# Kernel tuning notes

Hardware: AMD Instinct MI355X
Metric: run time of the kernel (lower is better)

## Reference

```python
import jax, jax.numpy as jnp
import numpy as np

B = 4096          # graphs (frames)
NPG = 22          # players per frame
N = B * NPG       # total nodes
E = B * NPG * (NPG - 1)
D_BB = 256        # backbone_dout == GRNN hidden
D_NODE = 128      # raw node feature dim
D_PROJ = 256      # cfg.proj_dout
D_GIN = 64        # glob_din
D_GOUT = 128      # cfg.glob_dout
D_IN = D_BB + D_PROJ  # GRNN input dim = 512


def setup_inputs() -> dict:
    key = jax.random.key(0)
    ks = jax.random.split(key, 24)
    def w(k, shape):
        return jax.random.normal(k, shape, jnp.float32) * 0.05
    inp = {
        "z": jax.random.normal(ks[0], (N, D_BB), jnp.float32),
        "u": jax.random.normal(ks[1], (B, D_GIN), jnp.float32),
        "x": jax.random.normal(ks[2], (N, D_NODE), jnp.float32),
        # edge_index is unused math-wise because GConvGRU is built with K=1 ChebConvs
        "edge_index": jax.random.randint(ks[3], (2, E), 0, N, dtype=jnp.int32),
        "batch": jnp.repeat(jnp.arange(B, dtype=jnp.int32), NPG),
        "batch_size": B,
        "prev_h": jax.random.normal(ks[4], (N, D_BB), jnp.float32),
        # fusion params
        "w_proj": w(ks[5], (D_NODE, D_PROJ)), "b_proj": jnp.zeros((D_PROJ,), jnp.float32),
        "w_glob": w(ks[6], (D_GIN, D_GOUT)), "b_glob": jnp.zeros((D_GOUT,), jnp.float32),
        # GConvGRU (K=1 ChebConv == linear) gate params: update z, reset r, candidate h
        "W_xz": w(ks[7], (D_IN, D_BB)),  "b_xz": jnp.zeros((D_BB,), jnp.float32),
        "W_hz": w(ks[8], (D_BB, D_BB)),  "b_hz": jnp.zeros((D_BB,), jnp.float32),
        "W_xr": w(ks[9], (D_IN, D_BB)),  "b_xr": jnp.zeros((D_BB,), jnp.float32),
        "W_hr": w(ks[10], (D_BB, D_BB)), "b_hr": jnp.zeros((D_BB,), jnp.float32),
        "W_xh": w(ks[11], (D_IN, D_BB)), "b_xh": jnp.zeros((D_BB,), jnp.float32),
        "W_hh": w(ks[12], (D_BB, D_BB)), "b_hh": jnp.zeros((D_BB,), jnp.float32),
    }
    return inp


def reference(z, u, x, edge_index, batch, batch_size, prev_h,
              w_proj, b_proj, w_glob, b_glob,
              W_xz, b_xz, W_hz, b_hz,
              W_xr, b_xr, W_hr, b_hr,
              W_xh, b_xh, W_hh, b_hh):
    # --- GraphGlobalFusion: mean readout + relu(Linear(u)) + concat ---
    sums = jax.ops.segment_sum(z, batch, num_segments=batch_size)            # [B, D_BB]
    cnts = jax.ops.segment_sum(jnp.ones((z.shape[0], 1), z.dtype), batch,
                               num_segments=batch_size)                      # [B, 1]
    graph_emb = sums / jnp.maximum(cnts, 1.0)
    glob_emb = jax.nn.relu(u @ w_glob + b_glob)                              # [B, D_GOUT]
    fused = jnp.concatenate([graph_emb, glob_emb], axis=-1)                  # [B, D_BB+D_GOUT]

    # --- node mode: raw feature projection, then GConvGRU (K=1 -> linear gates) ---
    x_proj = jax.nn.relu(x @ w_proj + b_proj)                                # [N, D_PROJ]
    xin = jnp.concatenate([z, x_proj], axis=-1)                              # [N, D_IN]
    Z = jax.nn.sigmoid(xin @ W_xz + b_xz + prev_h @ W_hz + b_hz)
    R = jax.nn.sigmoid(xin @ W_xr + b_xr + prev_h @ W_hr + b_hr)
    H_tilde = jnp.tanh(xin @ W_xh + b_xh + (prev_h * R) @ W_hh + b_hh)
    h = Z * prev_h + (1.0 - Z) * H_tilde                                     # [N, D_BB]
    return (fused, h)
```

## Files before the change

### kernel.cpp

```cpp
#include <hip/hip_runtime.h>
#include <hip/hip_bf16.h>

#define NNODES 90112
#define BGRAPH 4096
#define NPG 22
#define DBB 256
#define DNODE 128
#define DPROJ 256
#define DGIN 64
#define DGOUT 128

#define WTG_OFF   32768
#define WTHH_OFF  622592
#define WS_BF16_ELEMS 688128

typedef __attribute__((ext_vector_type(8))) short bf16x8;
typedef __attribute__((ext_vector_type(4))) short bf16x4;
typedef __attribute__((ext_vector_type(4))) float f32x4;

__device__ __forceinline__ short f2bf(float f) {
  __hip_bfloat16 h = __float2bfloat16(f);
  return *reinterpret_cast<short*>(&h);
}
__device__ __forceinline__ float bf2f(short s) {
  union { unsigned int u; float f; } c;
  c.u = ((unsigned int)(unsigned short)s) << 16;
  return c.f;
}
__device__ __forceinline__ float fsig(float xv) {
  return __fdividef(1.0f, 1.0f + __expf(-xv));
}
__device__ __forceinline__ float ftanh(float xv) {
  return 1.0f - __fdividef(2.0f, __expf(2.0f * xv) + 1.0f);
}
__device__ __forceinline__ bf16x8 pack8(f32x4 a, f32x4 b) {
  bf16x8 o;
  o[0]=f2bf(a[0]); o[1]=f2bf(a[1]); o[2]=f2bf(a[2]); o[3]=f2bf(a[3]);
  o[4]=f2bf(b[0]); o[5]=f2bf(b[1]); o[6]=f2bf(b[2]); o[7]=f2bf(b[3]);
  return o;
}

#define DMA16(gsrc, ldst)                                                        \
  __builtin_amdgcn_global_load_lds(                                              \
      (const __attribute__((address_space(1))) void*)(gsrc),                     \
      (__attribute__((address_space(3))) void*)(ldst), 16, 0, 0)

#define GLF(dst, p) asm volatile("global_load_dwordx4 %0, %1, off"               \
                                 : "=&v"(dst) : "v"(p) : "memory")

template<int N>
__device__ __forceinline__ void vmwaitN() {
  static_assert(N >= 0 && N <= 8, "vmcnt range");
  if constexpr (N == 0) asm volatile("s_waitcnt vmcnt(0)" ::: "memory");
  else if constexpr (N == 1) asm volatile("s_waitcnt vmcnt(1)" ::: "memory");
  else if constexpr (N == 2) asm volatile("s_waitcnt vmcnt(2)" ::: "memory");
  else if constexpr (N == 3) asm volatile("s_waitcnt vmcnt(3)" ::: "memory");
  else if constexpr (N == 4) asm volatile("s_waitcnt vmcnt(4)" ::: "memory");
  else if constexpr (N == 5) asm volatile("s_waitcnt vmcnt(5)" ::: "memory");
  else if constexpr (N == 6) asm volatile("s_waitcnt vmcnt(6)" ::: "memory");
  else if constexpr (N == 7) asm volatile("s_waitcnt vmcnt(7)" ::: "memory");
  else asm volatile("s_waitcnt vmcnt(8)" ::: "memory");
  __builtin_amdgcn_sched_barrier(0);
}
#define LBAR() do { asm volatile("s_waitcnt lgkmcnt(0)" ::: "memory");           \
                    __builtin_amdgcn_s_barrier(); } while (0)

__global__ void pack_weights(const float* __restrict__ w_proj,
                             const float* __restrict__ W_xz, const float* __restrict__ W_hz,
                             const float* __restrict__ W_xr, const float* __restrict__ W_hr,
                             const float* __restrict__ W_xh, const float* __restrict__ W_hh,
                             const float* __restrict__ b_xz, const float* __restrict__ b_hz,
                             const float* __restrict__ b_xr, const float* __restrict__ b_hr,
                             const float* __restrict__ b_xh, const float* __restrict__ b_hh,
                             __hip_bfloat16* __restrict__ wsb, float* __restrict__ wsf) {
  int i = blockIdx.x * 256 + threadIdx.x;
  if (i < 32768) {
    int c = i >> 7, k = i & 127;
    wsb[i] = __float2bfloat16(w_proj[k * DPROJ + c]);
  } else if (i < WTHH_OFF) {
    int j = i - WTG_OFF;
    int kc  = j / 24576;
    int rem = j - kc * 24576;
    int ct  = rem >> 9;
    int q   = rem & 511;
    int l   = q >> 3, e = q & 7;
    int l15 = l & 15, kg = l >> 4;
    int k   = kc * 32 + kg * 8 + e;
    int g   = ct >> 4;
    int c   = (ct & 15) * 16 + l15;
    float v;
    if (g == 0)      v = (k < 512) ? W_xz[k * 256 + c] : W_hz[(k - 512) * 256 + c];
    else if (g == 1) v = (k < 512) ? W_xr[k * 256 + c] : W_hr[(k - 512) * 256 + c];
    else             v = (k < 512) ? W_xh[k * 256 + c] : 0.0f;
    wsb[i] = __float2bfloat16(v);
  } else if (i < WS_BF16_ELEMS) {
    int j = i - WTHH_OFF;
    int kc  = j >> 13;
    int rem = j & 8191;
    int ct  = rem >> 9;
    int q   = rem & 511;
    int l   = q >> 3, e = q & 7;
    int l15 = l & 15, kg = l >> 4;
    int k   = kc * 32 + kg * 8 + e;
    int c   = ct * 16 + l15;
    wsb[i] = __float2bfloat16(W_hh[k * 256 + c]);
  }
  if (i < 256) {
    wsf[i]       = b_xz[i] + b_hz[i];
    wsf[256 + i] = b_xr[i] + b_hr[i];
    wsf[512 + i] = b_xh[i] + b_hh[i];
  }
}

__global__ void fused_head(const float* __restrict__ z, const float* __restrict__ u,
                           const float* __restrict__ w_glob, const float* __restrict__ b_glob,
                           float* __restrict__ out) {
  int b = blockIdx.x;
  int t = threadIdx.x;
  __shared__ float us[DGIN];
  if (t < DGIN) us[t] = u[b * DGIN + t];
  __syncthreads();
  const float* zb = z + (size_t)b * NPG * DBB;
  #pragma unroll
  for (int half = 0; half < 2; ++half) {
    int c = t + half * 128;
    float s = 0.f;
    #pragma unroll
    for (int r = 0; r < NPG; ++r) s += zb[r * DBB + c];
    out[(size_t)b * 384 + c] = s * (1.0f / NPG);
  }
  float acc = b_glob[t];
  #pragma unroll
  for (int k = 0; k < DGIN; ++k) acc += us[k] * w_glob[k * DGOUT + t];
  out[(size_t)b * 384 + 256 + t] = fmaxf(acc, 0.f);
}

#define MFMA16(a, b, c) __builtin_amdgcn_mfma_f32_16x16x32_bf16(a, b, c, 0, 0, 0)

template<int KC>
__device__ __forceinline__ void gstep(
    const __hip_bfloat16* __restrict__ wpk, __hip_bfloat16* Wb,
    const __hip_bfloat16* Av, const __hip_bfloat16* XP,
    int l15, int lg, int wid, int lane,
    f32x4 (&accz)[4], f32x4 (&accr)[4], f32x4 (&acch)[4]) {
  constexpr bool has_h = (KC < 16);
  constexpr int NW = (KC <= 8) ? 3
                   : (KC == 9 || KC == 10 || KC == 12 || KC == 13) ? 5
                   : (KC == 11 || KC == 14) ? 3
                   : (KC <= 22) ? 2 : 0;
  const __hip_bfloat16* ab = (KC >= 8 && KC < 16) ? XP : Av;
  const int gk = (KC & 7) * 4 + lg;
  bf16x8 act[4];
  #pragma unroll
  for (int rt = 0; rt < 4; ++rt) {
    const int row = rt * 16 + l15;
    act[rt] = *(const bf16x8*)(ab + row * 256 + ((gk ^ (row & 7)) * 8));
  }
  vmwaitN<NW>();
  bf16x8 wz = *(const bf16x8*)&Wb[((KC & 1) * 3 + 0) * 8192 + wid * 512 + lane * 8];
  bf16x8 wr = *(const bf16x8*)&Wb[((KC & 1) * 3 + 1) * 8192 + wid * 512 + lane * 8];
  bf16x8 wh;
  if constexpr (has_h)
    wh = *(const bf16x8*)&Wb[((KC & 1) * 3 + 2) * 8192 + wid * 512 + lane * 8];
  __builtin_amdgcn_s_setprio(1);
  #pragma unroll
  for (int rt = 0; rt < 4; ++rt) {
    accz[rt] = MFMA16(wz, act[rt], accz[rt]);
    accr[rt] = MFMA16(wr, act[rt], accr[rt]);
    if constexpr (has_h) acch[rt] = MFMA16(wh, act[rt], acch[rt]);
  }
  __builtin_amdgcn_s_setprio(0);
  if constexpr (KC + 2 <= 23) {
    constexpr int ns = ((KC + 2) < 16) ? 3 : 2;
    #pragma unroll
    for (int g = 0; g < 3; ++g)
      if (g < ns)
        DMA16(wpk + (((size_t)(KC + 2) * 48 + g * 16 + wid) * 64 + lane) * 8,
              Wb + (((KC + 2) & 1) * 3 + g) * 8192 + wid * 512);
  }
}

template<int S>
__device__ __forceinline__ void hstep(
    const __hip_bfloat16* __restrict__ hpk, __hip_bfloat16* Wb, __hip_bfloat16* XP,
    int l15, int lg, int wid, int lane, f32x4 (&acch)[4]) {
  constexpr int NW = (S <= 5) ? 2 : (S == 6) ? 1 : 0;
  bf16x8 act[4];
  #pragma unroll
  for (int rt = 0; rt < 4; ++rt) {
    const int row = rt * 16 + l15;
    const int gk = S * 4 + lg;
    act[rt] = *(const bf16x8*)&XP[row * 256 + ((gk ^ (row & 7)) * 8)];
  }
  vmwaitN<NW>();
  bf16x8 w = *(const bf16x8*)&Wb[(S % 4) * 8192 + wid * 512 + lane * 8];
  __builtin_amdgcn_s_setprio(1);
  #pragma unroll
  for (int rt = 0; rt < 4; ++rt) acch[rt] = MFMA16(w, act[rt], acch[rt]);
  __builtin_amdgcn_s_setprio(0);
  if constexpr (S + 3 <= 7)
    DMA16(hpk + (((size_t)(S + 3) * 16 + wid) * 64 + lane) * 8,
          Wb + ((S + 3) % 4) * 8192 + wid * 512);
}

__global__ __launch_bounds__(1024)
void grnn_main(const float* __restrict__ z, const float* __restrict__ x,
               const float* __restrict__ prev_h, const float* __restrict__ b_proj,
               const __hip_bfloat16* __restrict__ wsb, const float* __restrict__ wsf,
               float* __restrict__ h_out) {
  __shared__ __align__(16) __hip_bfloat16 Wb[6 * 8192];
  __shared__ __align__(16) __hip_bfloat16 Av[64 * 256];
  __shared__ __align__(16) __hip_bfloat16 XP[64 * 256];

  const int r0   = blockIdx.x * 64;
  const int tid  = threadIdx.x;
  const int wid  = tid >> 6;
  const int lane = tid & 63;
  const int l15  = lane & 15;
  const int lg   = lane >> 4;
  const int c0   = wid * 16;
  const int cgrp = (c0 >> 3) + (lg >> 1);
  const int lgl  = (lg & 1) * 4;
  const int prow = tid >> 4;
  const int pg   = tid & 15;

  const __hip_bfloat16* wpk = wsb + WTG_OFF;
  const __hip_bfloat16* hpk = wsb + WTHH_OFF;

  {
    const float* p = x + (size_t)(r0 + prow) * DNODE + pg * 8;
    f32x4 f0 = *(const f32x4*)p;
    f32x4 f1 = *(const f32x4*)(p + 4);
    *(bf16x8*)&XP[prow * 128 + ((pg ^ (prow & 7)) * 8)] = pack8(f0, f1);
  }
  __syncthreads();

  f32x4 z0, z1, z2, z3;
  {
    const float* zb = z + (size_t)(r0 + prow) * DBB + pg * 16;
    z0 = *(const f32x4*)zb;       z1 = *(const f32x4*)(zb + 4);
    z2 = *(const f32x4*)(zb + 8); z3 = *(const f32x4*)(zb + 12);
  }
  f32x4 accp[4] = {};
  {
    const __hip_bfloat16* wp0 = wsb + (size_t)(c0 + l15) * DNODE + lg * 8;
    #pragma unroll
    for (int kb = 0; kb < 4; ++kb) {
      bf16x8 wp = *(const bf16x8*)(wp0 + kb * 32);
      const int gk = kb * 4 + lg;
      bf16x8 act[4];
      #pragma unroll
      for (int rt = 0; rt < 4; ++rt) {
        const int row = rt * 16 + l15;
        act[rt] = *(const bf16x8*)&XP[row * 128 + ((gk ^ (row & 7)) * 8)];
      }
      __builtin_amdgcn_s_setprio(1);
      #pragma unroll
      for (int rt = 0; rt < 4; ++rt)
        accp[rt] = MFMA16(wp, act[rt], accp[rt]);
      __builtin_amdgcn_s_setprio(0);
    }
  }
  #pragma unroll
  for (int c = 0; c < 2; ++c)
    #pragma unroll
    for (int g = 0; g < 3; ++g)
      DMA16(wpk + (((size_t)c * 48 + g * 16 + wid) * 64 + lane) * 8,
            Wb + ((c & 1) * 3 + g) * 8192 + wid * 512);
  LBAR();
  {
    float4 bp4 = *(const float4*)&b_proj[c0 + lg * 4];
    #pragma unroll
    for (int rt = 0; rt < 4; ++rt) {
      int r = rt * 16 + l15;
      bf16x4 o;
      o[0] = f2bf(fmaxf(accp[rt][0] + bp4.x, 0.f));
      o[1] = f2bf(fmaxf(accp[rt][1] + bp4.y, 0.f));
      o[2] = f2bf(fmaxf(accp[rt][2] + bp4.z, 0.f));
      o[3] = f2bf(fmaxf(accp[rt][3] + bp4.w, 0.f));
      *(bf16x4*)&XP[r * 256 + ((cgrp ^ (r & 7)) * 8) + lgl] = o;
    }
  }
  *(bf16x8*)&Av[prow * 256 + (((2 * pg) ^ (prow & 7)) * 8)]     = pack8(z0, z1);
  *(bf16x8*)&Av[prow * 256 + (((2 * pg + 1) ^ (prow & 7)) * 8)] = pack8(z2, z3);
  LBAR();

  f32x4 accz[4] = {}, accr[4] = {}, acch[4] = {};
  const float* phb = prev_h + (size_t)(r0 + prow) * DBB + pg * 8;
  f32x4 pa0, pa1, pb0, pb1;
  #define GS(K) gstep<K>(wpk, Wb, Av, XP, l15, lg, wid, lane, accz, accr, acch)
  GS(0); GS(1); GS(2); GS(3); GS(4); GS(5); GS(6); GS(7);
  LBAR();
  GS(8);
  GLF(pa0, phb); GLF(pa1, phb + 4);
  GS(9); GS(10);
  vmwaitN<6>();
  *(bf16x8*)&Av[prow * 256 + ((pg ^ (prow & 7)) * 8)] = pack8(pa0, pa1);
  GS(11);
  GLF(pb0, phb + 128); GLF(pb1, phb + 132);
  GS(12); GS(13);
  vmwaitN<6>();
  *(bf16x8*)&Av[prow * 256 + (((16 + pg) ^ (prow & 7)) * 8)] = pack8(pb0, pb1);
  GS(14); GS(15);
  LBAR();
  GS(16); GS(17); GS(18); GS(19); GS(20); GS(21); GS(22); GS(23);
  #undef GS

  #pragma unroll
  for (int s = 0; s < 3; ++s)
    DMA16(hpk + (((size_t)s * 16 + wid) * 64 + lane) * 8, Wb + (s % 4) * 8192 + wid * 512);
  {
    float4 br4 = *(const float4*)&wsf[256 + c0 + lg * 4];
    #pragma unroll
    for (int rt = 0; rt < 4; ++rt) {
      int r = rt * 16 + l15;
      int off = r * 256 + ((cgrp ^ (r & 7)) * 8) + lgl;
      bf16x4 p4 = *(const bf16x4*)&Av[off];
      bf16x4 o;
      o[0] = f2bf(bf2f(p4[0]) * fsig(accr[rt][0] + br4.x));
      o[1] = f2bf(bf2f(p4[1]) * fsig(accr[rt][1] + br4.y));
      o[2] = f2bf(bf2f(p4[2]) * fsig(accr[rt][2] + br4.z));
      o[3] = f2bf(bf2f(p4[3]) * fsig(accr[rt][3] + br4.w));
      *(bf16x4*)&XP[off] = o;
    }
  }
  LBAR();

  #define HS(S) hstep<S>(hpk, Wb, XP, l15, lg, wid, lane, acch)
  HS(0); HS(1); HS(2); HS(3); HS(4); HS(5); HS(6); HS(7);
  #undef HS

  {
    float4 bz4 = *(const float4*)&wsf[c0 + lg * 4];
    float4 bh4 = *(const float4*)&wsf[512 + c0 + lg * 4];
    #pragma unroll
    for (int rt = 0; rt < 4; ++rt) {
      int r = rt * 16 + l15;
      bf16x4 p4 = *(const bf16x4*)&Av[r * 256 + ((cgrp ^ (r & 7)) * 8) + lgl];
      f32x4 hv;
      float zg = fsig(accz[rt][0] + bz4.x);
      hv[0] = zg * bf2f(p4[0]) + (1.f - zg) * ftanh(acch[rt][0] + bh4.x);
      zg = fsig(accz[rt][1] + bz4.y);
      hv[1] = zg * bf2f(p4[1]) + (1.f - zg) * ftanh(acch[rt][1] + bh4.y);
      zg = fsig(accz[rt][2] + bz4.z);
      hv[2] = zg * bf2f(p4[2]) + (1.f - zg) * ftanh(acch[rt][2] + bh4.z);
      zg = fsig(accz[rt][3] + bz4.w);
      hv[3] = zg * bf2f(p4[3]) + (1.f - zg) * ftanh(acch[rt][3] + bh4.w);
      *(f32x4*)&h_out[(size_t)(r0 + r) * DBB + c0 + lg * 4] = hv;
    }
  }
}

extern "C" void kernel_launch(void* const* d_in, const int* in_sizes, int n_in,
                              void* d_out, int out_size, void* d_ws, size_t ws_size,
                              hipStream_t stream) {
  const float* z      = (const float*)d_in[0];
  const float* u      = (const float*)d_in[1];
  const float* x      = (const float*)d_in[2];
  const float* prev_h = (const float*)d_in[6];
  const float* w_proj = (const float*)d_in[7];
  const float* b_proj = (const float*)d_in[8];
  const float* w_glob = (const float*)d_in[9];
  const float* b_glob = (const float*)d_in[10];
  const float* W_xz   = (const float*)d_in[11];
  const float* b_xz   = (const float*)d_in[12];
  const float* W_hz   = (const float*)d_in[13];
  const float* b_hz   = (const float*)d_in[14];
  const float* W_xr   = (const float*)d_in[15];
  const float* b_xr   = (const float*)d_in[16];
  const float* W_hr   = (const float*)d_in[17];
  const float* b_hr   = (const float*)d_in[18];
  const float* W_xh   = (const float*)d_in[19];
  const float* b_xh   = (const float*)d_in[20];
  const float* W_hh   = (const float*)d_in[21];
  const float* b_hh   = (const float*)d_in[22];

  __hip_bfloat16* wsb = (__hip_bfloat16*)d_ws;
  float* wsf = (float*)((char*)d_ws + (size_t)WS_BF16_ELEMS * 2);

  float* fused = (float*)d_out;
  float* h_out = fused + (size_t)BGRAPH * 384;

  pack_weights<<<dim3(WS_BF16_ELEMS / 256), dim3(256), 0, stream>>>(
      w_proj, W_xz, W_hz, W_xr, W_hr, W_xh, W_hh,
      b_xz, b_hz, b_xr, b_hr, b_xh, b_hh, wsb, wsf);

  fused_head<<<dim3(BGRAPH), dim3(128), 0, stream>>>(z, u, w_glob, b_glob, fused);

  grnn_main<<<dim3(NNODES / 64), dim3(1024), 0, stream>>>(
      z, x, prev_h, b_proj, wsb, wsf, h_out);
}
```

Before: 195.9 us.

## Fuse graph mean readout into GRNN kernel using staged bf16 tile and atomics

The per-graph mean of z is now computed inside grnn_main from the bf16 z tile already staged in shared memory and accumulated into the fused output with atomicAdd. The head kernel only zero-initialises that region and computes the global MLP. This removes a second full read of z from global memory. In exchange the sums are taken over bf16-rounded values, which lowers precision, and graphs that straddle tile boundaries need float atomics, which makes the summation order nondeterministic.

```diff
diff --git a/kernel.cpp b/kernel.cpp
--- a/kernel.cpp
+++ b/kernel.cpp
@@ -17,6 +17,7 @@
 typedef __attribute__((ext_vector_type(8))) short bf16x8;
 typedef __attribute__((ext_vector_type(4))) short bf16x4;
 typedef __attribute__((ext_vector_type(4))) float f32x4;
+typedef __attribute__((ext_vector_type(2))) float f32x2;
 
 __device__ __forceinline__ short f2bf(float f) {
   __hip_bfloat16 h = __float2bfloat16(f);
@@ -112,23 +113,16 @@
   }
 }
 
-__global__ void fused_head(const float* __restrict__ z, const float* __restrict__ u,
-                           const float* __restrict__ w_glob, const float* __restrict__ b_glob,
-                           float* __restrict__ out) {
+__global__ void head_init(const float* __restrict__ u,
+                          const float* __restrict__ w_glob, const float* __restrict__ b_glob,
+                          float* __restrict__ out) {
   int b = blockIdx.x;
   int t = threadIdx.x;
   __shared__ float us[DGIN];
   if (t < DGIN) us[t] = u[b * DGIN + t];
+  f32x2 zz = {0.f, 0.f};
+  *(f32x2*)&out[(size_t)b * 384 + t * 2] = zz;
   __syncthreads();
-  const float* zb = z + (size_t)b * NPG * DBB;
-  #pragma unroll
-  for (int half = 0; half < 2; ++half) {
-    int c = t + half * 128;
-    float s = 0.f;
-    #pragma unroll
-    for (int r = 0; r < NPG; ++r) s += zb[r * DBB + c];
-    out[(size_t)b * 384 + c] = s * (1.0f / NPG);
-  }
   float acc = b_glob[t];
   #pragma unroll
   for (int k = 0; k < DGIN; ++k) acc += us[k] * w_glob[k * DGOUT + t];
@@ -207,7 +201,7 @@
 void grnn_main(const float* __restrict__ z, const float* __restrict__ x,
                const float* __restrict__ prev_h, const float* __restrict__ b_proj,
                const __hip_bfloat16* __restrict__ wsb, const float* __restrict__ wsf,
-               float* __restrict__ h_out) {
+               float* __restrict__ fused, float* __restrict__ h_out) {
   __shared__ __align__(16) __hip_bfloat16 Wb[6 * 8192];
   __shared__ __align__(16) __hip_bfloat16 Av[64 * 256];
   __shared__ __align__(16) __hip_bfloat16 XP[64 * 256];
@@ -284,6 +278,23 @@
   *(bf16x8*)&Av[prow * 256 + (((2 * pg) ^ (prow & 7)) * 8)]     = pack8(z0, z1);
   *(bf16x8*)&Av[prow * 256 + (((2 * pg + 1) ^ (prow & 7)) * 8)] = pack8(z2, z3);
   LBAR();
+
+  {
+    const int gl = tid >> 8;
+    const int c  = tid & 255;
+    const int g  = r0 / NPG + gl;
+    if (g < BGRAPH) {
+      int lo = g * NPG - r0;      if (lo < 0) lo = 0;
+      int hi = g * NPG + NPG - r0; if (hi > 64) hi = 64;
+      if (lo < hi) {
+        const int cg = c >> 3, ce = c & 7;
+        float s = 0.f;
+        for (int row = lo; row < hi; ++row)
+          s += bf2f(*(const short*)&Av[row * 256 + (((cg ^ (row & 7)) << 3) + ce)]);
+        atomicAdd(&fused[(size_t)g * 384 + c], s * (1.0f / NPG));
+      }
+    }
+  }
 
   f32x4 accz[4] = {}, accr[4] = {}, acch[4] = {};
   const float* phb = prev_h + (size_t)(r0 + prow) * DBB + pg * 8;
@@ -385,8 +396,8 @@
       w_proj, W_xz, W_hz, W_xr, W_hr, W_xh, W_hh,
       b_xz, b_hz, b_xr, b_hr, b_xh, b_hh, wsb, wsf);
 
-  fused_head<<<dim3(BGRAPH), dim3(128), 0, stream>>>(z, u, w_glob, b_glob, fused);
+  head_init<<<dim3(BGRAPH), dim3(128), 0, stream>>>(u, w_glob, b_glob, fused);
 
   grnn_main<<<dim3(NNODES / 64), dim3(1024), 0, stream>>>(
-      z, x, prev_h, b_proj, wsb, wsf, h_out);
-}
+      z, x, prev_h, b_proj, wsb, wsf, fused, h_out);
+}
```

Measured after the change: 208.6 us. 6.4% more time.

## Compute per-graph z partial sums inside GRNN kernel from LDS-staged z

Applied to the files above, without the earlier changes.

The graph mean readout no longer re-reads z from global memory in a separate kernel. The GRNN kernel sums the bf16 z rows it has already staged in shared memory into per-block, per-graph partial sums in workspace, and a small head kernel combines at most two partials per graph. This saves a full pass over z (about 92 MB of fp32 reads) but computes the mean from bf16-rounded z, which adds some precision error. It also adds a serial shared-memory reduction step inside the main kernel.

```diff
diff --git a/kernel.cpp b/kernel.cpp
--- a/kernel.cpp
+++ b/kernel.cpp
@@ -9,14 +9,19 @@
 #define DPROJ 256
 #define DGIN 64
 #define DGOUT 128
+#define NBLK (NNODES / 64)
 
 #define WTG_OFF   32768
 #define WTHH_OFF  622592
 #define WS_BF16_ELEMS 688128
+#define WS2_BYTE_OFF ((size_t)WS_BF16_ELEMS * 2 + 768 * 4)
+#define WS2_BYTES    ((size_t)NBLK * 4 * 256 * 4)
+#define WS_NEED      (WS2_BYTE_OFF + WS2_BYTES)
 
 typedef __attribute__((ext_vector_type(8))) short bf16x8;
 typedef __attribute__((ext_vector_type(4))) short bf16x4;
 typedef __attribute__((ext_vector_type(4))) float f32x4;
+typedef __attribute__((ext_vector_type(2))) float f32x2;
 
 __device__ __forceinline__ short f2bf(float f) {
   __hip_bfloat16 h = __float2bfloat16(f);
@@ -135,6 +140,33 @@
   out[(size_t)b * 384 + 256 + t] = fmaxf(acc, 0.f);
 }
 
+__global__ void head2(const float* __restrict__ u,
+                      const float* __restrict__ w_glob, const float* __restrict__ b_glob,
+                      const float* __restrict__ ws2, float* __restrict__ out) {
+  int b = blockIdx.x;
+  int t = threadIdx.x;
+  __shared__ float us[DGIN];
+  if (t < DGIN) us[t] = u[b * DGIN + t];
+  __syncthreads();
+  const int rlo = b * NPG, rhi = b * NPG + NPG - 1;
+  const int b0 = rlo >> 6, b1 = rhi >> 6;
+  const int gl0 = b - (b0 * 64) / NPG;
+  #pragma unroll
+  for (int half = 0; half < 2; ++half) {
+    int c = t + half * 128;
+    float s = ws2[((size_t)b0 * 4 + gl0) * 256 + c];
+    if (b1 != b0) {
+      const int gl1 = b - (b1 * 64) / NPG;
+      s += ws2[((size_t)b1 * 4 + gl1) * 256 + c];
+    }
+    out[(size_t)b * 384 + c] = s * (1.0f / NPG);
+  }
+  float acc = b_glob[t];
+  #pragma unroll
+  for (int k = 0; k < DGIN; ++k) acc += us[k] * w_glob[k * DGOUT + t];
+  out[(size_t)b * 384 + 256 + t] = fmaxf(acc, 0.f);
+}
+
 #define MFMA16(a, b, c) __builtin_amdgcn_mfma_f32_16x16x32_bf16(a, b, c, 0, 0, 0)
 
 template<int KC>
@@ -207,7 +239,7 @@
 void grnn_main(const float* __restrict__ z, const float* __restrict__ x,
                const float* __restrict__ prev_h, const float* __restrict__ b_proj,
                const __hip_bfloat16* __restrict__ wsb, const float* __restrict__ wsf,
-               float* __restrict__ h_out) {
+               float* __restrict__ ws2, float* __restrict__ h_out) {
   __shared__ __align__(16) __hip_bfloat16 Wb[6 * 8192];
   __shared__ __align__(16) __hip_bfloat16 Av[64 * 256];
   __shared__ __align__(16) __hip_bfloat16 XP[64 * 256];
@@ -284,6 +316,26 @@
   *(bf16x8*)&Av[prow * 256 + (((2 * pg) ^ (prow & 7)) * 8)]     = pack8(z0, z1);
   *(bf16x8*)&Av[prow * 256 + (((2 * pg + 1) ^ (prow & 7)) * 8)] = pack8(z2, z3);
   LBAR();
+
+  if (ws2 != nullptr && tid < 512) {
+    const int gl = tid >> 7;
+    const int cp = tid & 127;
+    const int g  = r0 / NPG + gl;
+    float s0 = 0.f, s1 = 0.f;
+    if (g < BGRAPH) {
+      int lo = g * NPG - r0;       if (lo < 0) lo = 0;
+      int hi = g * NPG + NPG - r0; if (hi > 64) hi = 64;
+      const int c  = 2 * cp;
+      const int cg = c >> 3, ce = c & 7;
+      for (int row = lo; row < hi; ++row) {
+        unsigned int v = *(const unsigned int*)&Av[row * 256 + (((cg ^ (row & 7)) << 3) + ce)];
+        s0 += bf2f((short)(v & 0xffff));
+        s1 += bf2f((short)(v >> 16));
+      }
+    }
+    f32x2 o = { s0, s1 };
+    *(f32x2*)&ws2[((size_t)blockIdx.x * 4 + gl) * 256 + 2 * cp] = o;
+  }
 
   f32x4 accz[4] = {}, accr[4] = {}, acch[4] = {};
   const float* phb = prev_h + (size_t)(r0 + prow) * DBB + pg * 8;
@@ -381,12 +433,21 @@
   float* fused = (float*)d_out;
   float* h_out = fused + (size_t)BGRAPH * 384;
 
+  const bool big_ws = (ws_size >= WS_NEED);
+  float* ws2 = big_ws ? (float*)((char*)d_ws + WS2_BYTE_OFF) : nullptr;
+
   pack_weights<<<dim3(WS_BF16_ELEMS / 256), dim3(256), 0, stream>>>(
       w_proj, W_xz, W_hz, W_xr, W_hr, W_xh, W_hh,
       b_xz, b_hz, b_xr, b_hr, b_xh, b_hh, wsb, wsf);
 
-  fused_head<<<dim3(BGRAPH), dim3(128), 0, stream>>>(z, u, w_glob, b_glob, fused);
-
-  grnn_main<<<dim3(NNODES / 64), dim3(1024), 0, stream>>>(
-      z, x, prev_h, b_proj, wsb, wsf, h_out);
-}
+  if (!big_ws) {
+    fused_head<<<dim3(BGRAPH), dim3(128), 0, stream>>>(z, u, w_glob, b_glob, fused);
+  }
+
+  grnn_main<<<dim3(NBLK), dim3(1024), 0, stream>>>(
+      z, x, prev_h, b_proj, wsb, wsf, ws2, h_out);
+
+  if (big_ws) {
+    head2<<<dim3(BGRAPH), dim3(128), 0, stream>>>(u, w_glob, b_glob, ws2, fused);
+  }
+}
```

Measured after the change: 208.9 us. 6.6% more time.
